# Performance work log

Measured on AMD Instinct MI355X. Metric: run time of the kernel, lower is better.

## Reference

```python
import jax, jax.numpy as jnp
import numpy as np

V, D, E, N, Dd, Dc, NL, B, L = 50280, 1024, 2048, 16, 64, 4, 2, 2, 1024
EPS = 1e-5


def rmsnorm(x, w):
    return x * jax.lax.rsqrt(jnp.mean(x * x, axis=-1, keepdims=True) + EPS) * w


def setup_inputs() -> dict:
    key = jax.random.key(0)
    ks = jax.random.split(key, 18)
    n = jax.random.normal
    inp = {
        "input_ids": jax.random.randint(ks[0], (B, L), 0, V),
        "embedding": n(ks[1], (V, D), jnp.float32) * 0.02,
        "lm_head_w": n(ks[2], (V, D), jnp.float32) * 0.02,
        "norm_w": jnp.ones((D,), jnp.float32),
        # stacked per-layer params (leading dim = n_layer)
        "l_norm_w": jnp.ones((NL, D), jnp.float32),
        "l_skip_w": n(ks[3], (NL, E, D), jnp.float32) / np.sqrt(D),
        "l_in_w": n(ks[4], (NL, E, D), jnp.float32) / np.sqrt(D),
        "l_conv_w": n(ks[5], (NL, E, 1, Dc), jnp.float32) / np.sqrt(Dc),
        "l_conv_b": jnp.zeros((NL, E), jnp.float32),
        "l_Wd1": n(ks[6], (NL, Dd, E), jnp.float32) / np.sqrt(E),
        "l_Wd2_w": n(ks[7], (NL, E, Dd), jnp.float32) / np.sqrt(Dd),
        "l_Wd2_b": n(ks[8], (NL, E), jnp.float32) * 0.1 - 4.0,  # small dt init
        "l_WB": n(ks[9], (NL, N, E), jnp.float32) / np.sqrt(E),
        "l_WC": n(ks[10], (NL, N, E), jnp.float32) / np.sqrt(E),
        "l_A_log": jnp.log(jax.random.uniform(ks[11], (NL, E, N), jnp.float32, 0.5, 1.2)),
        "l_WD": jnp.ones((NL, E), jnp.float32),
        "l_out_w": n(ks[12], (NL, D, E), jnp.float32) / np.sqrt(E),
    }
    return inp


def mamba_layer(resid, norm_w, skip_w, in_w, conv_w, conv_b, Wd1, Wd2_w, Wd2_b,
                WB, WC, A_log, WD, out_w):
    x = rmsnorm(resid, norm_w)                      # [B,L,D]
    skip = x @ skip_w.T                             # [B,L,E]
    x = x @ in_w.T                                  # [B,L,E]
    # depthwise causal conv (pad D_conv-1 on left == pad both + slice [:L])
    xc = jax.lax.conv_general_dilated(
        x.transpose(0, 2, 1), conv_w, (1,), [(Dc - 1, 0)],
        feature_group_count=E, dimension_numbers=("NCH", "OIH", "NCH"))
    x = (xc + conv_b[None, :, None]).transpose(0, 2, 1)  # [B,L,E]
    x = jax.nn.silu(x)

    delta = jax.nn.softplus((x @ Wd1.T) @ Wd2_w.T + Wd2_b)  # [B,L,E]
    A = -jnp.exp(A_log)                                      # [E,N]
    A_bar = jnp.exp(delta[..., None] * A)                    # [B,L,E,N]
    Bt = x @ WB.T                                            # [B,L,N]
    Ct = x @ WC.T                                            # [B,L,N]
    Bx = (delta * x)[..., None] * Bt[:, :, None, :]          # [B,L,E,N]

    def step(h, inp):
        Ab_t, Bx_t, C_t = inp                                # [B,E,N],[B,E,N],[B,N]
        h = Ab_t * h + Bx_t
        y = jnp.einsum("ben,bn->be", h, C_t)
        return h, y

    h0 = jnp.zeros((B, E, N), x.dtype)
    _, ys = jax.lax.scan(step, h0,
                         (A_bar.transpose(1, 0, 2, 3), Bx.transpose(1, 0, 2, 3),
                          Ct.transpose(1, 0, 2)))
    y = ys.transpose(1, 0, 2)                                # [B,L,E]
    y = y + x * WD
    y = y * jax.nn.silu(skip)
    return resid + y @ out_w.T


def reference(input_ids, embedding, lm_head_w, norm_w, l_norm_w, l_skip_w, l_in_w,
              l_conv_w, l_conv_b, l_Wd1, l_Wd2_w, l_Wd2_b, l_WB, l_WC, l_A_log,
              l_WD, l_out_w):
    resid = embedding[input_ids]                             # [B,L,D]
    for i in range(NL):
        resid = mamba_layer(resid, l_norm_w[i], l_skip_w[i], l_in_w[i],
                            l_conv_w[i], l_conv_b[i], l_Wd1[i], l_Wd2_w[i],
                            l_Wd2_b[i], l_WB[i], l_WC[i], l_A_log[i], l_WD[i],
                            l_out_w[i])
    resid = rmsnorm(resid, norm_w)
    return resid @ lm_head_w.T                               # [B,L,V]
```

## Files before the change

### kernel.cpp

```cpp
#include <hip/hip_runtime.h>

typedef unsigned short u16;
using bf16x8 = __attribute__((ext_vector_type(8))) __bf16;
using f32x4  = __attribute__((ext_vector_type(4))) float;

typedef const void __attribute__((address_space(1))) gvoid_t;
typedef void __attribute__((address_space(3))) lvoid_t;

#define NL 2
#define Bd 2
#define Ld 1024
#define Dd_ 1024
#define Ed 2048
#define Nd 16
#define TOK (Bd*Ld)
#define VPAD 50432
#define VREAL 50280
#define NCHUNK 16
#define CLEN 64
#define XLD 4096

__device__ __forceinline__ u16 f2bf(float f) {
    union { float f; unsigned u; } v; v.f = f;
    unsigned u = v.u;
    unsigned r = (u + 0x7fffu + ((u >> 16) & 1u)) >> 16;
    return (u16)r;
}
__device__ __forceinline__ float siluf(float x) { return x / (1.f + __expf(-x)); }
__device__ __forceinline__ float softplusf(float z) {
    return (z > 15.f) ? z : log1pf(__expf(z));
}

__global__ void k_convert_all(const float* __restrict__ lmw, const float* __restrict__ lskip,
                              const float* __restrict__ linw, const float* __restrict__ loutw,
                              const float* __restrict__ lWd2, const float* __restrict__ lWd1,
                              const float* __restrict__ lWB, const float* __restrict__ lWC,
                              u16* __restrict__ lm_bf, u16* __restrict__ wsi_bf,
                              u16* __restrict__ wout_bf, u16* __restrict__ wd2_bf,
                              u16* __restrict__ wsml_bf) {
    int g = blockIdx.x * 256 + threadIdx.x;
    const float* src = nullptr; u16* dst = nullptr;
    if (g < 12910592) {
        dst = lm_bf + (size_t)g * 4;
        if (g < 12871680) src = lmw + (size_t)g * 4;
    } else if (g < 15007744) {
        int i = g - 12910592;
        int layer = i >> 20;
        int within = i & 1048575;
        int mat = within >> 19;
        int idx = within & 524287;
        src = (mat ? linw : lskip) + ((size_t)layer << 21) + ((size_t)idx * 4);
        dst = wsi_bf + ((size_t)layer << 22) + ((size_t)mat << 21) + ((size_t)idx * 4);
    } else if (g < 16056320) {
        int i = g - 15007744;
        src = loutw + (size_t)i * 4; dst = wout_bf + (size_t)i * 4;
    } else if (g < 16121856) {
        int i = g - 16056320;
        src = lWd2 + (size_t)i * 4; dst = wd2_bf + (size_t)i * 4;
    } else {
        int i = g - 16121856;
        int layer = i >> 16;
        int j = i & 65535;
        int col = (j * 4) & 2047;
        int r = (j * 4) >> 11;
        const float* s2 = nullptr;
        if (r < 64) s2 = lWd1 + ((size_t)layer * 64 + r) * 2048;
        else if (r < 80) s2 = lWB + ((size_t)layer * 16 + (r - 64)) * 2048;
        else if (r < 96) s2 = lWC + ((size_t)layer * 16 + (r - 80)) * 2048;
        dst = wsml_bf + ((size_t)layer << 18) + (size_t)j * 4;
        if (s2) src = s2 + col;
    }
    ushort4 o;
    if (src) {
        float4 v = *(const float4*)src;
        o.x = f2bf(v.x); o.y = f2bf(v.y); o.z = f2bf(v.z); o.w = f2bf(v.w);
    } else { o.x = o.y = o.z = o.w = 0; }
    *(ushort4*)dst = o;
}

__global__ void k_embed_norm(const int* __restrict__ ids, const float* __restrict__ emb,
                             const float* __restrict__ w, float* __restrict__ resid,
                             u16* __restrict__ out) {
    int tk = blockIdx.x, tid = threadIdx.x;
    int id = ids[tk];
    float4 v = *(const float4*)&emb[(size_t)id * Dd_ + tid * 4];
    *(float4*)&resid[(size_t)tk * Dd_ + tid * 4] = v;
    float ss = v.x * v.x + v.y * v.y + v.z * v.z + v.w * v.w;
    #pragma unroll
    for (int m = 32; m; m >>= 1) ss += __shfl_xor(ss, m);
    __shared__ float red[4];
    if ((tid & 63) == 0) red[tid >> 6] = ss;
    __syncthreads();
    ss = red[0] + red[1] + red[2] + red[3];
    float rs = rsqrtf(ss * (1.f / 1024.f) + 1e-5f);
    float4 wv = *(const float4*)&w[tid * 4];
    ushort4 o;
    o.x = f2bf(v.x * rs * wv.x); o.y = f2bf(v.y * rs * wv.y);
    o.z = f2bf(v.z * rs * wv.z); o.w = f2bf(v.w * rs * wv.w);
    *(ushort4*)&out[(size_t)tk * Dd_ + tid * 4] = o;
}

__global__ void k_add2_norm(const float* __restrict__ part, float* __restrict__ resid,
                            const float* __restrict__ w, u16* __restrict__ out) {
    int tk = blockIdx.x, tid = threadIdx.x;
    size_t i4 = (size_t)tk * Dd_ + tid * 4;
    float4 r = *(const float4*)&resid[i4];
    float4 a = *(const float4*)&part[i4];
    float4 b = *(const float4*)&part[(size_t)TOK * Dd_ + i4];
    r.x += a.x + b.x; r.y += a.y + b.y; r.z += a.z + b.z; r.w += a.w + b.w;
    *(float4*)&resid[i4] = r;
    float ss = r.x * r.x + r.y * r.y + r.z * r.z + r.w * r.w;
    #pragma unroll
    for (int m = 32; m; m >>= 1) ss += __shfl_xor(ss, m);
    __shared__ float red[4];
    if ((tid & 63) == 0) red[tid >> 6] = ss;
    __syncthreads();
    ss = red[0] + red[1] + red[2] + red[3];
    float rs = rsqrtf(ss * (1.f / 1024.f) + 1e-5f);
    float4 wv = *(const float4*)&w[tid * 4];
    ushort4 o;
    o.x = f2bf(r.x * rs * wv.x); o.y = f2bf(r.y * rs * wv.y);
    o.z = f2bf(r.z * rs * wv.z); o.w = f2bf(r.w * rs * wv.w);
    *(ushort4*)&out[(size_t)tk * Dd_ + tid * 4] = o;
}

__global__ void k_conv_silu(const float* __restrict__ xin, const float* __restrict__ cw,
                            const float* __restrict__ cb, float* __restrict__ xout,
                            u16* __restrict__ xbf) {
    int blk = blockIdx.x;
    int tk = blk >> 1;
    int e0 = ((blk & 1) << 10) + threadIdx.x * 4;
    int b = tk >> 10, l = tk & 1023;
    float4 w0 = *(const float4*)&cw[(size_t)(e0 + 0) * 4];
    float4 w1 = *(const float4*)&cw[(size_t)(e0 + 1) * 4];
    float4 w2 = *(const float4*)&cw[(size_t)(e0 + 2) * 4];
    float4 w3 = *(const float4*)&cw[(size_t)(e0 + 3) * 4];
    float4 bv = *(const float4*)&cb[e0];
    float a0 = bv.x, a1 = bv.y, a2 = bv.z, a3 = bv.w;
    const float* wp0 = (const float*)&w0; const float* wp1 = (const float*)&w1;
    const float* wp2 = (const float*)&w2; const float* wp3 = (const float*)&w3;
    #pragma unroll
    for (int k = 0; k < 4; ++k) {
        int ll = l - 3 + k;
        if (ll < 0) continue;
        float4 xv = *(const float4*)&xin[((size_t)(b * 1024 + ll)) * XLD + e0];
        a0 = fmaf(xv.x, wp0[k], a0); a1 = fmaf(xv.y, wp1[k], a1);
        a2 = fmaf(xv.z, wp2[k], a2); a3 = fmaf(xv.w, wp3[k], a3);
    }
    a0 = siluf(a0); a1 = siluf(a1); a2 = siluf(a2); a3 = siluf(a3);
    float4 o; o.x = a0; o.y = a1; o.z = a2; o.w = a3;
    *(float4*)&xout[(size_t)tk * Ed + e0] = o;
    ushort4 ob; ob.x = f2bf(a0); ob.y = f2bf(a1); ob.z = f2bf(a2); ob.w = f2bf(a3);
    *(ushort4*)&xbf[(size_t)tk * Ed + e0] = ob;
}

__global__ void k_reduce_xs(const float* __restrict__ part, float* __restrict__ xs,
                            u16* __restrict__ xsbf) {
    size_t i4 = ((size_t)blockIdx.x * 256 + threadIdx.x) * 4;
    float4 s = *(const float4*)&part[i4];
    #pragma unroll
    for (int c = 1; c < 8; ++c) {
        float4 v = *(const float4*)&part[(size_t)c * TOK * 128 + i4];
        s.x += v.x; s.y += v.y; s.z += v.z; s.w += v.w;
    }
    *(float4*)&xs[i4] = s;
    ushort4 o; o.x = f2bf(s.x); o.y = f2bf(s.y); o.z = f2bf(s.z); o.w = f2bf(s.w);
    *(ushort4*)&xsbf[i4] = o;
}

__global__ void k_scan_pass1(const float* __restrict__ delta, const float* __restrict__ x,
                             const float* __restrict__ xs, const float* __restrict__ A_log,
                             float* __restrict__ sumd, float* __restrict__ Hc) {
    __shared__ float sBt[CLEN][16];
    int t = blockIdx.x * 256 + threadIdx.x;
    int e = t & (Ed - 1);
    int cb = t >> 11;
    int b = cb & 1, c = cb >> 1;
    int rowbase = b * 1024 + c * CLEN;
    {
        int f = threadIdx.x * 4;
        int row = f >> 4, cc = f & 15;
        float4 v = *(const float4*)&xs[(size_t)(rowbase + row) * 128 + 64 + cc];
        *(float4*)&sBt[row][cc] = v;
    }
    __syncthreads();
    float dA[16], h[16];
    #pragma unroll
    for (int n = 0; n < 16; ++n) { dA[n] = -__expf(A_log[e * 16 + n]); h[n] = 0.f; }
    float sd = 0.f;
    for (int l = 0; l < CLEN; ++l) {
        size_t row = (size_t)rowbase + l;
        float dlt = delta[row * Ed + e];
        float xv  = x[row * Ed + e];
        sd += dlt;
        float dx = dlt * xv;
        float4 bt0 = *(const float4*)&sBt[l][0];
        float4 bt1 = *(const float4*)&sBt[l][4];
        float4 bt2 = *(const float4*)&sBt[l][8];
        float4 bt3 = *(const float4*)&sBt[l][12];
        float bts[16] = {bt0.x,bt0.y,bt0.z,bt0.w, bt1.x,bt1.y,bt1.z,bt1.w,
                         bt2.x,bt2.y,bt2.z,bt2.w, bt3.x,bt3.y,bt3.z,bt3.w};
        #pragma unroll
        for (int n = 0; n < 16; ++n) {
            float a = __expf(dA[n] * dlt);
            h[n] = fmaf(a, h[n], dx * bts[n]);
        }
    }
    size_t gg = (size_t)cb * Ed + e;
    #pragma unroll
    for (int n = 0; n < 16; ++n) Hc[gg * 16 + n] = h[n];
    sumd[gg] = sd;
}

__global__ void k_scan_pass2(const float* __restrict__ delta, const float* __restrict__ x,
                             const float* __restrict__ xs, const float* __restrict__ A_log,
                             const float* __restrict__ sumd, const float* __restrict__ Hc,
                             const float* __restrict__ WD,
                             const float* __restrict__ skipg, u16* __restrict__ ybf) {
    __shared__ float sBC[CLEN][32];
    int t = blockIdx.x * 256 + threadIdx.x;
    int e = t & (Ed - 1);
    int cb = t >> 11;
    int b = cb & 1, c = cb >> 1;
    int rowbase = b * 1024 + c * CLEN;
    {
        int f = threadIdx.x * 8;
        int row = f >> 5, cc = f & 31;
        float4 v0 = *(const float4*)&xs[(size_t)(rowbase + row) * 128 + 64 + cc];
        float4 v1 = *(const float4*)&xs[(size_t)(rowbase + row) * 128 + 64 + cc + 4];
        *(float4*)&sBC[row][cc] = v0;
        *(float4*)&sBC[row][cc + 4] = v1;
    }
    __syncthreads();
    float dA[16], h[16];
    #pragma unroll
    for (int n = 0; n < 16; ++n) {
        dA[n] = -__expf(A_log[e * 16 + n]);
        h[n] = 0.f;
    }
    for (int cc = 0; cc < c; ++cc) {
        size_t g2 = ((size_t)(cc * Bd + b) * Ed + e);
        float sdc = sumd[g2];
        #pragma unroll
        for (int n = 0; n < 16; ++n)
            h[n] = fmaf(__expf(dA[n] * sdc), h[n], Hc[g2 * 16 + n]);
    }
    float wd = WD[e];
    for (int l = 0; l < CLEN; ++l) {
        size_t row = (size_t)rowbase + l;
        float dlt = delta[row * Ed + e];
        float xv  = x[row * Ed + e];
        float dx = dlt * xv;
        float4 b0 = *(const float4*)&sBC[l][0];
        float4 b1 = *(const float4*)&sBC[l][4];
        float4 b2 = *(const float4*)&sBC[l][8];
        float4 b3 = *(const float4*)&sBC[l][12];
        float4 c0 = *(const float4*)&sBC[l][16];
        float4 c1 = *(const float4*)&sBC[l][20];
        float4 c2 = *(const float4*)&sBC[l][24];
        float4 c3 = *(const float4*)&sBC[l][28];
        float bts[16] = {b0.x,b0.y,b0.z,b0.w, b1.x,b1.y,b1.z,b1.w,
                         b2.x,b2.y,b2.z,b2.w, b3.x,b3.y,b3.z,b3.w};
        float cts[16] = {c0.x,c0.y,c0.z,c0.w, c1.x,c1.y,c1.z,c1.w,
                         c2.x,c2.y,c2.z,c2.w, c3.x,c3.y,c3.z,c3.w};
        float y = 0.f;
        #pragma unroll
        for (int n = 0; n < 16; ++n) {
            float a = __expf(dA[n] * dlt);
            h[n] = fmaf(a, h[n], dx * bts[n]);
            y = fmaf(h[n], cts[n], y);
        }
        float yo = y + xv * wd;
        float sk = skipg[row * XLD + e];
        ybf[row * Ed + e] = f2bf(yo * siluf(sk));
    }
}

template<int EPI>
__global__ __launch_bounds__(256, 2)
void k_gemm_bt(const u16* __restrict__ A, int lda,
               const u16* __restrict__ B, int ldb,
               float* __restrict__ C, int ldc,
               const float* __restrict__ aux,
               int ntm, int Nstore, int Kc, size_t Cz) {
    __shared__ u16 lsA[2][128 * 32];
    __shared__ u16 lsB[2][128 * 32];
    int kz = blockIdx.z;
    A += (size_t)kz * Kc;
    B += (size_t)kz * Kc;
    C += (size_t)kz * Cz;
    int tid = threadIdx.x;
    int bid = blockIdx.x;
    int mt = bid % ntm, nt = bid / ntm;
    int mBase = mt * 128, nBase = nt * 128;
    int lane = tid & 63, wid = tid >> 6;
    int wr = wid >> 1, wc = wid & 1;

    f32x4 acc[4][4] = {};
    const u16* Ablk = A + (size_t)mBase * lda;
    const u16* Bblk = B + (size_t)nBase * ldb;
    int nk = Kc >> 5;

    auto stage = [&](int buf, int kt) {
        #pragma unroll
        for (int i = 0; i < 2; ++i) {
            int chunk = i * 256 + tid;
            int row = chunk >> 2;
            int kc  = (chunk & 3) << 3;
            const u16* ga = Ablk + (size_t)row * lda + (kt << 5) + kc;
            const u16* gb = Bblk + (size_t)row * ldb + (kt << 5) + kc;
            u16* la = &lsA[buf][(size_t)(i * 256 + wid * 64) * 8];
            u16* lb = &lsB[buf][(size_t)(i * 256 + wid * 64) * 8];
            __builtin_amdgcn_global_load_lds((gvoid_t*)ga, (lvoid_t*)la, 16, 0, 0);
            __builtin_amdgcn_global_load_lds((gvoid_t*)gb, (lvoid_t*)lb, 16, 0, 0);
        }
    };
    auto compute = [&](int buf) {
        bf16x8 af[4], bfr[4];
        const u16* baseA = lsA[buf];
        const u16* baseB = lsB[buf];
        int kq = (lane >> 4) << 3;
        int r  = lane & 15;
        #pragma unroll
        for (int mi = 0; mi < 4; ++mi)
            af[mi] = *(const bf16x8*)&baseA[(size_t)((wr * 64 + mi * 16 + r) * 32 + kq)];
        #pragma unroll
        for (int ni = 0; ni < 4; ++ni)
            bfr[ni] = *(const bf16x8*)&baseB[(size_t)((wc * 64 + ni * 16 + r) * 32 + kq)];
        #pragma unroll
        for (int mi = 0; mi < 4; ++mi)
            #pragma unroll
            for (int ni = 0; ni < 4; ++ni)
                acc[mi][ni] = __builtin_amdgcn_mfma_f32_16x16x32_bf16(af[mi], bfr[ni], acc[mi][ni], 0, 0, 0);
    };

    stage(0, 0);
    asm volatile("s_waitcnt vmcnt(0)" ::: "memory");
    __syncthreads();
    int cur = 0;
    for (int kt = 0; kt + 1 < nk; ++kt) {
        stage(cur ^ 1, kt + 1);
        compute(cur);
        asm volatile("s_waitcnt vmcnt(0)" ::: "memory");
        __syncthreads();
        cur ^= 1;
    }
    compute(cur);

    int rbase = (lane >> 4) * 4, ccol = lane & 15;
    #pragma unroll
    for (int mi = 0; mi < 4; ++mi) {
        #pragma unroll
        for (int ni = 0; ni < 4; ++ni) {
            int gc = nBase + wc * 64 + ni * 16 + ccol;
            if (gc < Nstore) {
                float bias = (EPI == 2) ? aux[gc] : 0.f;
                #pragma unroll
                for (int rr = 0; rr < 4; ++rr) {
                    int gr = mBase + wr * 64 + mi * 16 + rbase + rr;
                    size_t off = (size_t)gr * ldc + gc;
                    float v = acc[mi][ni][rr];
                    if (EPI == 2) v = softplusf(v + bias);
                    C[off] = v;
                }
            }
        }
    }
}

#define BAR()    asm volatile("s_barrier" ::: "memory")
#define WAITV2() asm volatile("s_waitcnt vmcnt(2)" ::: "memory")
#define WAITV0() asm volatile("s_waitcnt vmcnt(0)" ::: "memory")

#define STG(buf, mat, h, kt) { \
    const u16* _s0 = ((mat) ? srcB[(h)*2]     : srcA[(h)*2])     + (size_t)(kt) * 64; \
    const u16* _s1 = ((mat) ? srcB[(h)*2 + 1] : srcA[(h)*2 + 1]) + (size_t)(kt) * 64; \
    char* _d = (char*)&ls[buf][mat][0]; \
    __builtin_amdgcn_global_load_lds((gvoid_t*)_s0, (lvoid_t*)(_d + (h)*16384 + tid*16), 16, 0, 0); \
    __builtin_amdgcn_global_load_lds((gvoid_t*)_s1, (lvoid_t*)(_d + (h)*16384 + 8192 + tid*16), 16, 0, 0); }

#define QUAD(buf, kk, mih) { \
    const char* _pa = (const char*)&ls[buf][0][0]; \
    const char* _pb = (const char*)&ls[buf][1][0]; \
    bf16x8 _af[4], _bf[4]; \
    _Pragma("unroll") \
    for (int _m = 0; _m < 4; ++_m) \
        _af[_m] = *(const bf16x8*)(_pa + abase + ((mih)*4 + _m) * 2048 + (kk) * 1024); \
    _Pragma("unroll") \
    for (int _n = 0; _n < 4; ++_n) \
        _bf[_n] = *(const bf16x8*)(_pb + bbase + _n * 2048 + (kk) * 1024); \
    __builtin_amdgcn_s_setprio(1); \
    _Pragma("unroll") \
    for (int _m = 0; _m < 4; ++_m) \
        _Pragma("unroll") \
        for (int _n = 0; _n < 4; ++_n) \
            acc[(mih)*4 + _m][_n] = __builtin_amdgcn_mfma_f32_16x16x32_bf16(_af[_m], _bf[_n], acc[(mih)*4 + _m][_n], 0, 0, 0); \
    __builtin_amdgcn_s_setprio(0); }

__global__ __launch_bounds__(512, 2)
void k_gemm256(const u16* __restrict__ A, int lda,
               const u16* __restrict__ B, int ldb,
               float* __restrict__ C, int ldc,
               int ntm, int Nstore, int K) {
    __shared__ u16 ls[2][2][256 * 64];
    const int tid = threadIdx.x;
    const int lane = tid & 63, wid = tid >> 6;
    const int wr = wid >> 2, wc = wid & 3;

    int nwg = gridDim.x, bid = blockIdx.x;
    int q8 = nwg >> 3, r8 = nwg & 7;
    int xcd = bid & 7, linb = bid >> 3;
    int sb = (xcd < r8 ? xcd * (q8 + 1) : r8 * (q8 + 1) + (xcd - r8) * q8) + linb;
    int mt = sb % ntm, nt = sb / ntm;

    const u16* Ablk = A + (size_t)(mt * 256) * lda;
    const u16* Bblk = B + (size_t)(nt * 256) * ldb;

    const u16* srcA[4]; const u16* srcB[4];
    #pragma unroll
    for (int s = 0; s < 4; ++s) {
        int p = s * 8192 + tid * 16;
        int qq = p ^ (((p >> 9) & 1) << 5);
        int sub = qq >> 10, rin = (qq >> 6) & 15, cby = qq & 63;
        int row = ((sub >> 1) << 4) | rin;
        int col = ((((sub & 1) << 6) | cby)) >> 1;
        srcA[s] = Ablk + (size_t)row * lda + col;
        srcB[s] = Bblk + (size_t)row * ldb + col;
    }
    int l15 = lane & 15;
    int lowb = (l15 * 64 + ((lane >> 4) << 4)) ^ (((l15 >> 3) & 1) << 5);
    int abase = wr * 16384 + lowb;
    int bbase = wc * 8192  + lowb;

    f32x4 acc[8][4] = {};
    int nk = K >> 6, nit = nk >> 1;

    STG(0, 0, 0, 0); STG(0, 0, 1, 0); STG(0, 1, 0, 0); STG(0, 1, 1, 0);

    for (int i = 0; i < nit; ++i) {
        int t1 = 2 * i + 1, t2 = 2 * i + 2;
        bool more = (i + 1 < nit);
        STG(1, 0, 0, t1);
        WAITV2(); BAR();
        QUAD(0, 0, 0); BAR();
        STG(1, 0, 1, t1);
        QUAD(0, 0, 1); BAR();
        STG(1, 1, 0, t1);
        QUAD(0, 1, 0); BAR();
        STG(1, 1, 1, t1);
        QUAD(0, 1, 1); BAR();
        if (more) { STG(0, 0, 0, t2); WAITV2(); } else { WAITV0(); }
        BAR();
        QUAD(1, 0, 0); BAR();
        if (more) STG(0, 0, 1, t2);
        QUAD(1, 0, 1); BAR();
        if (more) STG(0, 1, 0, t2);
        QUAD(1, 1, 0); BAR();
        if (more) STG(0, 1, 1, t2);
        QUAD(1, 1, 1); BAR();
    }

    int rb = (lane >> 4) * 4, cc = lane & 15;
    int mrow = mt * 256 + wr * 128, ncol = nt * 256 + wc * 64;
    #pragma unroll
    for (int mi = 0; mi < 8; ++mi) {
        #pragma unroll
        for (int ni = 0; ni < 4; ++ni) {
            int gc = ncol + ni * 16 + cc;
            if (gc < Nstore) {
                #pragma unroll
                for (int rr = 0; rr < 4; ++rr) {
                    size_t off = (size_t)(mrow + mi * 16 + rb + rr) * ldc + gc;
                    C[off] = acc[mi][ni][rr];
                }
            }
        }
    }
}

extern "C" void kernel_launch(void* const* d_in, const int* in_sizes, int n_in,
                              void* d_out, int out_size, void* d_ws, size_t ws_size,
                              hipStream_t stream) {
    const int*   ids   = (const int*)d_in[0];
    const float* emb   = (const float*)d_in[1];
    const float* lmw   = (const float*)d_in[2];
    const float* normw = (const float*)d_in[3];
    const float* lnw   = (const float*)d_in[4];
    const float* lskip = (const float*)d_in[5];
    const float* linw  = (const float*)d_in[6];
    const float* lcw   = (const float*)d_in[7];
    const float* lcb   = (const float*)d_in[8];
    const float* lWd1  = (const float*)d_in[9];
    const float* lWd2  = (const float*)d_in[10];
    const float* lWd2b = (const float*)d_in[11];
    const float* lWB   = (const float*)d_in[12];
    const float* lWC   = (const float*)d_in[13];
    const float* lAlog = (const float*)d_in[14];
    const float* lWD   = (const float*)d_in[15];
    const float* loutw = (const float*)d_in[16];
    float* out = (float*)d_out;

    char* ws = (char*)d_ws;
    size_t off = 0;
    auto alloc = [&](size_t bytes) { char* p = ws + off; off += (bytes + 255) & ~(size_t)255; return p; };
    u16*   lm_bf    = (u16*)  alloc((size_t)VPAD * 1024 * 2);
    u16*   wsi_bf   = (u16*)  alloc((size_t)NL * 4096 * Dd_ * 2);
    u16*   wout_bf  = (u16*)  alloc((size_t)NL * Dd_ * Ed * 2);
    u16*   wd2_bf   = (u16*)  alloc((size_t)NL * Ed * 64 * 2);
    u16*   wsml_bf  = (u16*)  alloc((size_t)NL * 128 * Ed * 2);
    float* resid    = (float*)alloc((size_t)TOK * Dd_ * 4);
    u16*   xn_bf    = (u16*)  alloc((size_t)TOK * Dd_ * 2);
    float* xall     = (float*)alloc((size_t)TOK * XLD * 4);
    float* xf       = (float*)alloc((size_t)TOK * Ed * 4);
    u16*   xbf      = (u16*)  alloc((size_t)TOK * Ed * 2);
    float* xs       = (float*)alloc((size_t)TOK * 128 * 4);
    u16*   xs_bf    = (u16*)  alloc((size_t)TOK * 128 * 2);
    float* xs_part  = (float*)alloc((size_t)8 * TOK * 128 * 4);
    float* opart    = (float*)alloc((size_t)2 * TOK * Dd_ * 4);
    float* delta    = (float*)alloc((size_t)TOK * Ed * 4);
    float* sumd     = (float*)alloc((size_t)NCHUNK * Bd * Ed * 4);
    float* Hc       = (float*)alloc((size_t)NCHUNK * Bd * Ed * Nd * 4);
    u16*   ybf      = (u16*)  alloc((size_t)TOK * Ed * 2);
    (void)ws_size; (void)in_sizes; (void)n_in; (void)out_size;

    k_convert_all<<<63488, 256, 0, stream>>>(lmw, lskip, linw, loutw, lWd2, lWd1, lWB, lWC,
                                             lm_bf, wsi_bf, wout_bf, wd2_bf, wsml_bf);

    k_embed_norm<<<TOK, 256, 0, stream>>>(ids, emb, lnw, resid, xn_bf);

    for (int lyr = 0; lyr < NL; ++lyr) {
        const float* Alog = lAlog + (size_t)lyr * Ed * Nd;
        k_gemm_bt<0><<<dim3(16 * 32, 1, 1), 256, 0, stream>>>(xn_bf, Dd_,
            wsi_bf + (size_t)lyr * 4096 * Dd_, Dd_, xall, XLD, nullptr, 16, 4096, 1024, 0);
        k_conv_silu<<<TOK * 2, 256, 0, stream>>>(xall + Ed, lcw + (size_t)lyr * Ed * 4,
                                                 lcb + (size_t)lyr * Ed, xf, xbf);
        k_gemm_bt<0><<<dim3(16, 1, 8), 256, 0, stream>>>(xbf, Ed,
            wsml_bf + (size_t)lyr * 128 * Ed, Ed, xs_part, 128, nullptr, 16, 128, 256,
            (size_t)TOK * 128);
        k_reduce_xs<<<TOK * 128 / 4 / 256, 256, 0, stream>>>(xs_part, xs, xs_bf);
        k_gemm_bt<2><<<dim3(16 * 16, 1, 1), 256, 0, stream>>>(xs_bf, 128,
            wd2_bf + (size_t)lyr * Ed * 64, 64, delta, Ed, lWd2b + (size_t)lyr * Ed,
            16, Ed, 64, 0);
        k_scan_pass1<<<NCHUNK * Bd * Ed / 256, 256, 0, stream>>>(delta, xf, xs, Alog, sumd, Hc);
        k_scan_pass2<<<NCHUNK * Bd * Ed / 256, 256, 0, stream>>>(delta, xf, xs, Alog,
            sumd, Hc, lWD + (size_t)lyr * Ed, xall, ybf);
        k_gemm_bt<0><<<dim3(16 * 8, 1, 2), 256, 0, stream>>>(ybf, Ed,
            wout_bf + (size_t)lyr * Dd_ * Ed, Ed, opart, Dd_, nullptr, 16, Dd_, 1024,
            (size_t)TOK * Dd_);
        const float* nw = (lyr == NL - 1) ? normw : lnw + (size_t)(lyr + 1) * Dd_;
        k_add2_norm<<<TOK, 256, 0, stream>>>(opart, resid, nw, xn_bf);
    }

    k_gemm256<<<dim3(8 * (VPAD / 256), 1, 1), 512, 0, stream>>>(xn_bf, Dd_, lm_bf, Dd_,
        out, VREAL, 8, VREAL, 1024);
}
```

Before: 802.8 us.

## Store skip/in projections and conv output as bf16; widen weight conversion

The skip/in projection GEMM now writes bf16 through a new epilogue mode, and the conv, scan and gating kernels read bf16 activations. The separate fp32 conv output buffer is dropped, so the scan passes read the bf16 copy. This roughly halves activation traffic between these kernels. Separately, the weight conversion kernel now handles 8 elements per thread with 16-byte stores. The cost is lower precision for x, skip and the scan inputs, which could affect accuracy.

Result: faster. 784.6 us (-2.3%).

```diff
diff --git a/kernel.cpp b/kernel.cpp
--- a/kernel.cpp
+++ b/kernel.cpp
@@ -26,6 +26,12 @@
     unsigned r = (u + 0x7fffu + ((u >> 16) & 1u)) >> 16;
     return (u16)r;
 }
+__device__ __forceinline__ float bf2f(u16 u) {
+    union { unsigned u; float f; } v; v.u = ((unsigned)u) << 16; return v.f;
+}
+__device__ __forceinline__ unsigned pk2(float a, float b) {
+    return (unsigned)f2bf(a) | ((unsigned)f2bf(b) << 16);
+}
 __device__ __forceinline__ float siluf(float x) { return x / (1.f + __expf(-x)); }
 __device__ __forceinline__ float softplusf(float z) {
     return (z > 15.f) ? z : log1pf(__expf(z));
@@ -40,42 +46,44 @@
                               u16* __restrict__ wsml_bf) {
     int g = blockIdx.x * 256 + threadIdx.x;
     const float* src = nullptr; u16* dst = nullptr;
-    if (g < 12910592) {
-        dst = lm_bf + (size_t)g * 4;
-        if (g < 12871680) src = lmw + (size_t)g * 4;
-    } else if (g < 15007744) {
-        int i = g - 12910592;
-        int layer = i >> 20;
-        int within = i & 1048575;
-        int mat = within >> 19;
-        int idx = within & 524287;
-        src = (mat ? linw : lskip) + ((size_t)layer << 21) + ((size_t)idx * 4);
-        dst = wsi_bf + ((size_t)layer << 22) + ((size_t)mat << 21) + ((size_t)idx * 4);
-    } else if (g < 16056320) {
-        int i = g - 15007744;
-        src = loutw + (size_t)i * 4; dst = wout_bf + (size_t)i * 4;
-    } else if (g < 16121856) {
-        int i = g - 16056320;
-        src = lWd2 + (size_t)i * 4; dst = wd2_bf + (size_t)i * 4;
+    if (g < 6455296) {
+        dst = lm_bf + (size_t)g * 8;
+        if (g < 6435840) src = lmw + (size_t)g * 8;
+    } else if (g < 7503872) {
+        int i = g - 6455296;
+        int layer = i >> 19;
+        int within = i & 524287;
+        int mat = within >> 18;
+        int idx = within & 262143;
+        src = (mat ? linw : lskip) + ((size_t)layer << 21) + ((size_t)idx * 8);
+        dst = wsi_bf + ((size_t)layer << 22) + ((size_t)mat << 21) + ((size_t)idx * 8);
+    } else if (g < 8028160) {
+        int i = g - 7503872;
+        src = loutw + (size_t)i * 8; dst = wout_bf + (size_t)i * 8;
+    } else if (g < 8060928) {
+        int i = g - 8028160;
+        src = lWd2 + (size_t)i * 8; dst = wd2_bf + (size_t)i * 8;
     } else {
-        int i = g - 16121856;
-        int layer = i >> 16;
-        int j = i & 65535;
-        int col = (j * 4) & 2047;
-        int r = (j * 4) >> 11;
+        int i = g - 8060928;
+        int layer = i >> 15;
+        int j = i & 32767;
+        int col = (j * 8) & 2047;
+        int r = (j * 8) >> 11;
         const float* s2 = nullptr;
         if (r < 64) s2 = lWd1 + ((size_t)layer * 64 + r) * 2048;
         else if (r < 80) s2 = lWB + ((size_t)layer * 16 + (r - 64)) * 2048;
         else if (r < 96) s2 = lWC + ((size_t)layer * 16 + (r - 80)) * 2048;
-        dst = wsml_bf + ((size_t)layer << 18) + (size_t)j * 4;
+        dst = wsml_bf + ((size_t)layer << 18) + (size_t)j * 8;
         if (s2) src = s2 + col;
     }
-    ushort4 o;
+    uint4 o;
     if (src) {
-        float4 v = *(const float4*)src;
-        o.x = f2bf(v.x); o.y = f2bf(v.y); o.z = f2bf(v.z); o.w = f2bf(v.w);
+        float4 v0 = *(const float4*)src;
+        float4 v1 = *(const float4*)(src + 4);
+        o.x = pk2(v0.x, v0.y); o.y = pk2(v0.z, v0.w);
+        o.z = pk2(v1.x, v1.y); o.w = pk2(v1.z, v1.w);
     } else { o.x = o.y = o.z = o.w = 0; }
-    *(ushort4*)dst = o;
+    *(uint4*)dst = o;
 }
 
 __global__ void k_embed_norm(const int* __restrict__ ids, const float* __restrict__ emb,
@@ -124,9 +132,8 @@
     *(ushort4*)&out[(size_t)tk * Dd_ + tid * 4] = o;
 }
 
-__global__ void k_conv_silu(const float* __restrict__ xin, const float* __restrict__ cw,
-                            const float* __restrict__ cb, float* __restrict__ xout,
-                            u16* __restrict__ xbf) {
+__global__ void k_conv_silu(const u16* __restrict__ xin, const float* __restrict__ cw,
+                            const float* __restrict__ cb, u16* __restrict__ xbf) {
     int blk = blockIdx.x;
     int tk = blk >> 1;
     int e0 = ((blk & 1) << 10) + threadIdx.x * 4;
@@ -143,13 +150,11 @@
     for (int k = 0; k < 4; ++k) {
         int ll = l - 3 + k;
         if (ll < 0) continue;
-        float4 xv = *(const float4*)&xin[((size_t)(b * 1024 + ll)) * XLD + e0];
-        a0 = fmaf(xv.x, wp0[k], a0); a1 = fmaf(xv.y, wp1[k], a1);
-        a2 = fmaf(xv.z, wp2[k], a2); a3 = fmaf(xv.w, wp3[k], a3);
+        ushort4 xv = *(const ushort4*)&xin[((size_t)(b * 1024 + ll)) * XLD + e0];
+        a0 = fmaf(bf2f(xv.x), wp0[k], a0); a1 = fmaf(bf2f(xv.y), wp1[k], a1);
+        a2 = fmaf(bf2f(xv.z), wp2[k], a2); a3 = fmaf(bf2f(xv.w), wp3[k], a3);
     }
     a0 = siluf(a0); a1 = siluf(a1); a2 = siluf(a2); a3 = siluf(a3);
-    float4 o; o.x = a0; o.y = a1; o.z = a2; o.w = a3;
-    *(float4*)&xout[(size_t)tk * Ed + e0] = o;
     ushort4 ob; ob.x = f2bf(a0); ob.y = f2bf(a1); ob.z = f2bf(a2); ob.w = f2bf(a3);
     *(ushort4*)&xbf[(size_t)tk * Ed + e0] = ob;
 }
@@ -168,7 +173,7 @@
     *(ushort4*)&xsbf[i4] = o;
 }
 
-__global__ void k_scan_pass1(const float* __restrict__ delta, const float* __restrict__ x,
+__global__ void k_scan_pass1(const float* __restrict__ delta, const u16* __restrict__ x,
                              const float* __restrict__ xs, const float* __restrict__ A_log,
                              float* __restrict__ sumd, float* __restrict__ Hc) {
     __shared__ float sBt[CLEN][16];
@@ -191,7 +196,7 @@
     for (int l = 0; l < CLEN; ++l) {
         size_t row = (size_t)rowbase + l;
         float dlt = delta[row * Ed + e];
-        float xv  = x[row * Ed + e];
+        float xv  = bf2f(x[row * Ed + e]);
         sd += dlt;
         float dx = dlt * xv;
         float4 bt0 = *(const float4*)&sBt[l][0];
@@ -212,11 +217,11 @@
     sumd[gg] = sd;
 }
 
-__global__ void k_scan_pass2(const float* __restrict__ delta, const float* __restrict__ x,
+__global__ void k_scan_pass2(const float* __restrict__ delta, const u16* __restrict__ x,
                              const float* __restrict__ xs, const float* __restrict__ A_log,
                              const float* __restrict__ sumd, const float* __restrict__ Hc,
                              const float* __restrict__ WD,
-                             const float* __restrict__ skipg, u16* __restrict__ ybf) {
+                             const u16* __restrict__ skipg, u16* __restrict__ ybf) {
     __shared__ float sBC[CLEN][32];
     int t = blockIdx.x * 256 + threadIdx.x;
     int e = t & (Ed - 1);
@@ -249,7 +254,7 @@
     for (int l = 0; l < CLEN; ++l) {
         size_t row = (size_t)rowbase + l;
         float dlt = delta[row * Ed + e];
-        float xv  = x[row * Ed + e];
+        float xv  = bf2f(x[row * Ed + e]);
         float dx = dlt * xv;
         float4 b0 = *(const float4*)&sBC[l][0];
         float4 b1 = *(const float4*)&sBC[l][4];
@@ -271,7 +276,7 @@
             y = fmaf(h[n], cts[n], y);
         }
         float yo = y + xv * wd;
-        float sk = skipg[row * XLD + e];
+        float sk = bf2f(skipg[row * XLD + e]);
         ybf[row * Ed + e] = f2bf(yo * siluf(sk));
     }
 }
@@ -361,7 +366,8 @@
                     size_t off = (size_t)gr * ldc + gc;
                     float v = acc[mi][ni][rr];
                     if (EPI == 2) v = softplusf(v + bias);
-                    C[off] = v;
+                    if (EPI == 3) ((u16*)C)[off] = f2bf(v);
+                    else          C[off] = v;
                 }
             }
         }
@@ -510,8 +516,7 @@
     u16*   wsml_bf  = (u16*)  alloc((size_t)NL * 128 * Ed * 2);
     float* resid    = (float*)alloc((size_t)TOK * Dd_ * 4);
     u16*   xn_bf    = (u16*)  alloc((size_t)TOK * Dd_ * 2);
-    float* xall     = (float*)alloc((size_t)TOK * XLD * 4);
-    float* xf       = (float*)alloc((size_t)TOK * Ed * 4);
+    u16*   xall_bf  = (u16*)  alloc((size_t)TOK * XLD * 2);
     u16*   xbf      = (u16*)  alloc((size_t)TOK * Ed * 2);
     float* xs       = (float*)alloc((size_t)TOK * 128 * 4);
     u16*   xs_bf    = (u16*)  alloc((size_t)TOK * 128 * 2);
@@ -523,17 +528,18 @@
     u16*   ybf      = (u16*)  alloc((size_t)TOK * Ed * 2);
     (void)ws_size; (void)in_sizes; (void)n_in; (void)out_size;
 
-    k_convert_all<<<63488, 256, 0, stream>>>(lmw, lskip, linw, loutw, lWd2, lWd1, lWB, lWC,
+    k_convert_all<<<31744, 256, 0, stream>>>(lmw, lskip, linw, loutw, lWd2, lWd1, lWB, lWC,
                                              lm_bf, wsi_bf, wout_bf, wd2_bf, wsml_bf);
 
     k_embed_norm<<<TOK, 256, 0, stream>>>(ids, emb, lnw, resid, xn_bf);
 
     for (int lyr = 0; lyr < NL; ++lyr) {
         const float* Alog = lAlog + (size_t)lyr * Ed * Nd;
-        k_gemm_bt<0><<<dim3(16 * 32, 1, 1), 256, 0, stream>>>(xn_bf, Dd_,
-            wsi_bf + (size_t)lyr * 4096 * Dd_, Dd_, xall, XLD, nullptr, 16, 4096, 1024, 0);
-        k_conv_silu<<<TOK * 2, 256, 0, stream>>>(xall + Ed, lcw + (size_t)lyr * Ed * 4,
-                                                 lcb + (size_t)lyr * Ed, xf, xbf);
+        k_gemm_bt<3><<<dim3(16 * 32, 1, 1), 256, 0, stream>>>(xn_bf, Dd_,
+            wsi_bf + (size_t)lyr * 4096 * Dd_, Dd_, (float*)xall_bf, XLD, nullptr,
+            16, 4096, 1024, 0);
+        k_conv_silu<<<TOK * 2, 256, 0, stream>>>(xall_bf + Ed, lcw + (size_t)lyr * Ed * 4,
+                                                 lcb + (size_t)lyr * Ed, xbf);
         k_gemm_bt<0><<<dim3(16, 1, 8), 256, 0, stream>>>(xbf, Ed,
             wsml_bf + (size_t)lyr * 128 * Ed, Ed, xs_part, 128, nullptr, 16, 128, 256,
             (size_t)TOK * 128);
@@ -541,9 +547,9 @@
         k_gemm_bt<2><<<dim3(16 * 16, 1, 1), 256, 0, stream>>>(xs_bf, 128,
             wd2_bf + (size_t)lyr * Ed * 64, 64, delta, Ed, lWd2b + (size_t)lyr * Ed,
             16, Ed, 64, 0);
-        k_scan_pass1<<<NCHUNK * Bd * Ed / 256, 256, 0, stream>>>(delta, xf, xs, Alog, sumd, Hc);
-        k_scan_pass2<<<NCHUNK * Bd * Ed / 256, 256, 0, stream>>>(delta, xf, xs, Alog,
-            sumd, Hc, lWD + (size_t)lyr * Ed, xall, ybf);
+        k_scan_pass1<<<NCHUNK * Bd * Ed / 256, 256, 0, stream>>>(delta, xbf, xs, Alog, sumd, Hc);
+        k_scan_pass2<<<NCHUNK * Bd * Ed / 256, 256, 0, stream>>>(delta, xbf, xs, Alog,
+            sumd, Hc, lWD + (size_t)lyr * Ed, xall_bf, ybf);
         k_gemm_bt<0><<<dim3(16 * 8, 1, 2), 256, 0, stream>>>(ybf, Ed,
             wout_bf + (size_t)lyr * Dd_ * Ed, Ed, opart, Dd_, nullptr, 16, Dd_, 1024,
             (size_t)TOK * Dd_);
```
